# Optimization experiments

Measured on AMD Instinct MI355X. Metric: run time of the kernel, lower is better.

## Reference

```python
import jax, jax.numpy as jnp
import numpy as np
import math

N = 8192
DIM = 256

def setup_inputs() -> dict:
    key = jax.random.key(0)
    k1, k2, k3 = jax.random.split(key, 3)
    h = jax.random.normal(k1, (N, DIM), dtype=jnp.float32)
    # xavier_uniform with gain=1.414 for square [dim, dim] matrices
    gain = 1.414
    bound = gain * math.sqrt(6.0 / (DIM + DIM))
    Wq = jax.random.uniform(k2, (DIM, DIM), dtype=jnp.float32, minval=-bound, maxval=bound)
    Wk = jax.random.uniform(k3, (DIM, DIM), dtype=jnp.float32, minval=-bound, maxval=bound)
    return {"h": h, "Wq": Wq, "Wk": Wk}

def reference(h, Wq, Wk):
    dim = h.shape[1]
    q = h @ Wq                                   # [N, dim]
    k = h @ Wk                                   # [N, dim]
    e = (q @ k.T) / jnp.sqrt(jnp.asarray(dim, h.dtype))  # [N, N]
    attention = jax.nn.softmax(e, axis=1)        # row-wise softmax
    attention = attention.mean(axis=0)           # [N], column-mean over rows
    x = attention @ h                            # [dim]
    return x
```

## Files before the change

kernel.cpp:

```cpp
#include <hip/hip_runtime.h>
#include <cstdint>
#include <cstddef>


#define N_ROWS 8192
#define DIM    256

typedef __bf16 bf16x8 __attribute__((ext_vector_type(8)));
typedef unsigned short u16x8 __attribute__((ext_vector_type(8)));
typedef float f32x16 __attribute__((ext_vector_type(16)));

__device__ __forceinline__ uint16_t f2bf(float f) {
    uint32_t u = __float_as_uint(f);
    uint32_t r = (u + 0x7fffu + ((u >> 16) & 1u)) >> 16;
    return (uint16_t)r;
}

__device__ __forceinline__ float fexp2(float x) {
#if __has_builtin(__builtin_amdgcn_exp2f)
    return __builtin_amdgcn_exp2f(x);
#else
    return __expf(x * 0.69314718056f);
#endif
}

__device__ __forceinline__ void gld16(const void* gsrc, void* ldst) {
    __builtin_amdgcn_global_load_lds(
        (const __attribute__((address_space(1))) unsigned int*)gsrc,
        (__attribute__((address_space(3))) unsigned int*)ldst, 16, 0, 0);
}

__global__ __launch_bounds__(256) void proj_kernel(
        const float* __restrict__ h, const float* __restrict__ Wq,
        const float* __restrict__ Wk, uint16_t* __restrict__ qf,
        uint16_t* __restrict__ kf, float* __restrict__ l_arr,
        float* __restrict__ c_arr, float* __restrict__ out) {
    __shared__ alignas(16) uint16_t wb[256 * 128];
    const int tid = threadIdx.x, lane = tid & 63, wave = tid >> 6;
    const int which = blockIdx.x & 1;
    const int rt = blockIdx.x >> 1;

    if (blockIdx.x < 32)       l_arr[blockIdx.x * 256 + tid] = 0.0f;
    else if (blockIdx.x < 64)  c_arr[(blockIdx.x - 32) * 256 + tid] = 0.0f;
    else if (blockIdx.x == 64) out[tid] = 0.0f;

    const float* __restrict__ W = which ? Wk : Wq;
    uint16_t* __restrict__ dst = which ? kf : qf;
    const float scale = which ? 1.0f : (0.0625f * 1.44269504089f);

    {
        float* hb = (float*)wb;
        for (int i = tid; i < 2048; i += 256) {
            int r = i >> 6, c = (i & 63) * 4;
            float4 v = *(const float4*)&h[(size_t)(rt * 32 + r) * DIM + c];
            *(float4*)&hb[r * 260 + c] = v;
        }
    }
    __syncthreads();

    bf16x8 afrag[16];
    {
        const float* hb = (const float*)wb;
        const int r = lane & 31;
#pragma unroll
        for (int a0 = 0; a0 < 16; a0++) {
            const int c0 = a0 * 16 + (lane >> 5) * 8;
            float4 f0 = *(const float4*)&hb[r * 260 + c0];
            float4 f1 = *(const float4*)&hb[r * 260 + c0 + 4];
            u16x8 f;
            f[0] = f2bf(f0.x); f[1] = f2bf(f0.y); f[2] = f2bf(f0.z); f[3] = f2bf(f0.w);
            f[4] = f2bf(f1.x); f[5] = f2bf(f1.y); f[6] = f2bf(f1.z); f[7] = f2bf(f1.w);
            afrag[a0] = __builtin_bit_cast(bf16x8, f);
        }
    }

    for (int p = 0; p < 2; p++) {
        __syncthreads();
#pragma unroll
        for (int c = 0; c < 32; c++) {
            int f = c * 256 + tid;
            int k = f >> 5, nc = (f & 31) * 4;
            float4 w4 = *(const float4*)&W[(size_t)k * DIM + p * 128 + nc];
            ushort4 b;
            b.x = f2bf(w4.x); b.y = f2bf(w4.y); b.z = f2bf(w4.z); b.w = f2bf(w4.w);
            *(ushort4*)&wb[k * 128 + nc] = b;
        }
        __syncthreads();

        f32x16 acc;
#pragma unroll
        for (int i = 0; i < 16; i++) acc[i] = 0.0f;
        const int cl = wave * 32 + (lane & 31);
#pragma unroll
        for (int a0 = 0; a0 < 16; a0++) {
            const int kb = a0 * 16 + (lane >> 5) * 8;
            u16x8 f;
#pragma unroll
            for (int j = 0; j < 8; j++) f[j] = wb[(kb + j) * 128 + cl];
            acc = __builtin_amdgcn_mfma_f32_32x32x16_bf16(
                afrag[a0], __builtin_bit_cast(bf16x8, f), acc, 0, 0, 0);
        }
        __syncthreads();

        {
            uint16_t* rp = &wb[wave * 2048];
            const int dcl = lane & 31;
            const int a0o = dcl >> 4, hi = (dcl >> 3) & 1, j = dcl & 7;
            const int ilb = 4 * (lane >> 5);
#pragma unroll
            for (int reg = 0; reg < 16; reg++) {
                int il = ilb + (reg & 3) + 8 * (reg >> 2);
                rp[(size_t)((a0o * 64) + il + 32 * hi) * 8 + j] =
                    f2bf(acc[reg] * scale);
            }
            const uint4* rv = (const uint4*)rp;
            uint4* gp = (uint4*)(dst + (size_t)rt * 8192 +
                                 (size_t)(p * 8 + wave * 2) * 512);
            gp[lane * 2]     = rv[lane * 2];
            gp[lane * 2 + 1] = rv[lane * 2 + 1];
        }
    }
}

template <int MODE>
__global__ __launch_bounds__(256, 2) void qk_pass(
        const uint16_t* __restrict__ qf, const uint16_t* __restrict__ kf,
        float* __restrict__ l_arr, float* __restrict__ c_arr) {
    __shared__ alignas(16) uint16_t ktile[2][8192];
    __shared__ float c_lds[512];
    const int tid = threadIdx.x, lane = tid & 63, wave = tid >> 6;
    const int bid = blockIdx.x;
    const int cc = bid & 15, rb = bid >> 4;
    const int t0 = rb * 8 + wave * 2;
    const int row0 = t0 * 32;

    const uint4* qp = (const uint4*)qf;
    bf16x8 q0[16], q1[16];
#pragma unroll
    for (int a0 = 0; a0 < 16; a0++) {
        q0[a0] = __builtin_bit_cast(bf16x8, qp[(size_t)t0 * 1024 + a0 * 64 + lane]);
        q1[a0] = __builtin_bit_cast(bf16x8, qp[(size_t)(t0 + 1) * 1024 + a0 * 64 + lane]);
    }

    float rs0[16], rs1[16];
    float rr0[16], rr1[16];
    if (MODE == 0) {
#pragma unroll
        for (int r = 0; r < 16; r++) { rs0[r] = 0.0f; rs1[r] = 0.0f; }
    } else {
#pragma unroll
        for (int r = 0; r < 16; r++) {
            int ro = (r & 3) + 8 * (r >> 2) + 4 * (lane >> 5);
            rr0[r] = 1.0f / (8192.0f * l_arr[row0 + ro]);
            rr1[r] = 1.0f / (8192.0f * l_arr[row0 + 32 + ro]);
        }
        for (int i = tid; i < 512; i += 256) c_lds[i] = 0.0f;
    }

    const char* ksrc = (const char*)kf + (size_t)cc * 16 * 16384;

    {
        const char* s0 = ksrc + wave * 4096 + lane * 16;
        char* d0 = (char*)&ktile[0][0] + wave * 4096;
#pragma unroll
        for (int it = 0; it < 4; it++) gld16(s0 + it * 1024, d0 + it * 1024);
    }

    for (int t = 0; t < 16; t++) {
        __syncthreads();
        if (t < 15) {
            const char* sn = ksrc + (t + 1) * 16384 + wave * 4096 + lane * 16;
            char* dn = (char*)&ktile[(t + 1) & 1][0] + wave * 4096;
#pragma unroll
            for (int it = 0; it < 4; it++) gld16(sn + it * 1024, dn + it * 1024);
        }

        const uint16_t* kt = &ktile[t & 1][0];
        f32x16 acc0, acc1;
#pragma unroll
        for (int i = 0; i < 16; i++) { acc0[i] = 0.0f; acc1[i] = 0.0f; }
#pragma unroll
        for (int a0 = 0; a0 < 16; a0++) {
            bf16x8 b = __builtin_bit_cast(bf16x8,
                *(const u16x8*)&kt[(size_t)(a0 * 64 + lane) * 8]);
            acc0 = __builtin_amdgcn_mfma_f32_32x32x16_bf16(q0[a0], b, acc0, 0, 0, 0);
            acc1 = __builtin_amdgcn_mfma_f32_32x32x16_bf16(q1[a0], b, acc1, 0, 0, 0);
        }

        if (MODE == 0) {
#pragma unroll
            for (int r = 0; r < 16; r++) {
                rs0[r] += fexp2(acc0[r]);
                rs1[r] += fexp2(acc1[r]);
            }
        } else {
            float sv = 0.0f;
#pragma unroll
            for (int r = 0; r < 16; r++) {
                sv += fexp2(acc0[r]) * rr0[r];
                sv += fexp2(acc1[r]) * rr1[r];
            }
            sv += __shfl_xor(sv, 32);
            if (lane < 32) atomicAdd(&c_lds[t * 32 + lane], sv);
        }
    }

    if (MODE == 0) {
#pragma unroll
        for (int r = 0; r < 16; r++) {
            float v0 = rs0[r], v1 = rs1[r];
            v0 += __shfl_xor(v0, 1);  v0 += __shfl_xor(v0, 2);
            v0 += __shfl_xor(v0, 4);  v0 += __shfl_xor(v0, 8);
            v0 += __shfl_xor(v0, 16);
            v1 += __shfl_xor(v1, 1);  v1 += __shfl_xor(v1, 2);
            v1 += __shfl_xor(v1, 4);  v1 += __shfl_xor(v1, 8);
            v1 += __shfl_xor(v1, 16);
            if ((lane & 31) == 0) {
                int ro = (r & 3) + 8 * (r >> 2) + 4 * (lane >> 5);
                atomicAdd(&l_arr[row0 + ro], v0);
                atomicAdd(&l_arr[row0 + 32 + ro], v1);
            }
        }
    } else {
        __syncthreads();
        for (int i = tid; i < 512; i += 256)
            atomicAdd(&c_arr[cc * 512 + i], c_lds[i]);
    }
}

__global__ __launch_bounds__(256) void finish_kernel(
        const float* __restrict__ h, const float* __restrict__ c_arr,
        float* __restrict__ out) {
    const int d = threadIdx.x;
    const int j0 = blockIdx.x * 64;
    float acc = 0.0f;
    for (int j = j0; j < j0 + 64; j++) acc += c_arr[j] * h[(size_t)j * DIM + d];
    atomicAdd(&out[d], acc);
}

extern "C" void kernel_launch(void* const* d_in, const int* in_sizes, int n_in,
                              void* d_out, int out_size, void* d_ws, size_t ws_size,
                              hipStream_t stream) {
    const float* h  = (const float*)d_in[0];
    const float* Wq = (const float*)d_in[1];
    const float* Wk = (const float*)d_in[2];

    uint16_t* qf = (uint16_t*)d_ws;
    uint16_t* kf = qf + (size_t)N_ROWS * DIM;
    float* l_arr = (float*)((char*)d_ws + (size_t)8 * 1024 * 1024);
    float* c_arr = l_arr + N_ROWS;
    float* out = (float*)d_out;

    proj_kernel<<<512, 256, 0, stream>>>(h, Wq, Wk, qf, kf, l_arr, c_arr, out);
    qk_pass<0><<<512, 256, 0, stream>>>(qf, kf, l_arr, c_arr);
    qk_pass<1><<<512, 256, 0, stream>>>(qf, kf, l_arr, c_arr);
    finish_kernel<<<128, 256, 0, stream>>>(h, c_arr, out);
}
```

Before: 162.5 us.

## Restructure projection kernel to compute Q and K per block with direct W loads

The projection kernel now uses 128 blocks that each cover 64 rows of h, converting h to bf16 once in shared memory. Each block computes both the Q and K projections, and waves read W straight from global memory with per-element bf16 conversion instead of staging W through LDS with barriers. This cuts repeated h loads and barriers but replaces coalesced W staging with strided scalar global reads that rely on the cache. The finish kernel is also split into 256 blocks of 32 rows with an unrolled loop to raise parallelism.

```diff
diff --git a/kernel.cpp b/kernel.cpp
--- a/kernel.cpp
+++ b/kernel.cpp
@@ -35,87 +35,68 @@
         const float* __restrict__ Wk, uint16_t* __restrict__ qf,
         uint16_t* __restrict__ kf, float* __restrict__ l_arr,
         float* __restrict__ c_arr, float* __restrict__ out) {
-    __shared__ alignas(16) uint16_t wb[256 * 128];
+    __shared__ alignas(16) uint16_t hb16[64 * 264];
+    __shared__ alignas(16) uint16_t rep[4][1024];
     const int tid = threadIdx.x, lane = tid & 63, wave = tid >> 6;
-    const int which = blockIdx.x & 1;
-    const int rt = blockIdx.x >> 1;
-
-    if (blockIdx.x < 32)       l_arr[blockIdx.x * 256 + tid] = 0.0f;
-    else if (blockIdx.x < 64)  c_arr[(blockIdx.x - 32) * 256 + tid] = 0.0f;
-    else if (blockIdx.x == 64) out[tid] = 0.0f;
-
-    const float* __restrict__ W = which ? Wk : Wq;
-    uint16_t* __restrict__ dst = which ? kf : qf;
-    const float scale = which ? 1.0f : (0.0625f * 1.44269504089f);
-
-    {
-        float* hb = (float*)wb;
-        for (int i = tid; i < 2048; i += 256) {
-            int r = i >> 6, c = (i & 63) * 4;
-            float4 v = *(const float4*)&h[(size_t)(rt * 32 + r) * DIM + c];
-            *(float4*)&hb[r * 260 + c] = v;
-        }
+    const int bid = blockIdx.x;
+
+    if (bid < 32)       l_arr[bid * 256 + tid] = 0.0f;
+    else if (bid < 64)  c_arr[(bid - 32) * 256 + tid] = 0.0f;
+    else if (bid == 64) out[tid] = 0.0f;
+
+    for (int i = tid; i < 4096; i += 256) {
+        int r = i >> 6, c4 = (i & 63) * 4;
+        float4 v = *(const float4*)&h[(size_t)(bid * 64 + r) * DIM + c4];
+        ushort4 b;
+        b.x = f2bf(v.x); b.y = f2bf(v.y); b.z = f2bf(v.z); b.w = f2bf(v.w);
+        *(ushort4*)&hb16[r * 264 + c4] = b;
     }
     __syncthreads();
 
     bf16x8 afrag[16];
-    {
-        const float* hb = (const float*)wb;
-        const int r = lane & 31;
-#pragma unroll
-        for (int a0 = 0; a0 < 16; a0++) {
-            const int c0 = a0 * 16 + (lane >> 5) * 8;
-            float4 f0 = *(const float4*)&hb[r * 260 + c0];
-            float4 f1 = *(const float4*)&hb[r * 260 + c0 + 4];
-            u16x8 f;
-            f[0] = f2bf(f0.x); f[1] = f2bf(f0.y); f[2] = f2bf(f0.z); f[3] = f2bf(f0.w);
-            f[4] = f2bf(f1.x); f[5] = f2bf(f1.y); f[6] = f2bf(f1.z); f[7] = f2bf(f1.w);
-            afrag[a0] = __builtin_bit_cast(bf16x8, f);
-        }
-    }
-
-    for (int p = 0; p < 2; p++) {
-        __syncthreads();
-#pragma unroll
-        for (int c = 0; c < 32; c++) {
-            int f = c * 256 + tid;
-            int k = f >> 5, nc = (f & 31) * 4;
-            float4 w4 = *(const float4*)&W[(size_t)k * DIM + p * 128 + nc];
-            ushort4 b;
-            b.x = f2bf(w4.x); b.y = f2bf(w4.y); b.z = f2bf(w4.z); b.w = f2bf(w4.w);
-            *(ushort4*)&wb[k * 128 + nc] = b;
-        }
-        __syncthreads();
-
-        f32x16 acc;
-#pragma unroll
-        for (int i = 0; i < 16; i++) acc[i] = 0.0f;
-        const int cl = wave * 32 + (lane & 31);
-#pragma unroll
-        for (int a0 = 0; a0 < 16; a0++) {
-            const int kb = a0 * 16 + (lane >> 5) * 8;
-            u16x8 f;
-#pragma unroll
-            for (int j = 0; j < 8; j++) f[j] = wb[(kb + j) * 128 + cl];
-            acc = __builtin_amdgcn_mfma_f32_32x32x16_bf16(
-                afrag[a0], __builtin_bit_cast(bf16x8, f), acc, 0, 0, 0);
-        }
-        __syncthreads();
-
-        {
-            uint16_t* rp = &wb[wave * 2048];
+    const int lr = (wave >> 1) * 32 + (lane & 31);
+#pragma unroll
+    for (int a0 = 0; a0 < 16; a0++) {
+        int c0 = a0 * 16 + (lane >> 5) * 8;
+        afrag[a0] = __builtin_bit_cast(bf16x8, *(const u16x8*)&hb16[lr * 264 + c0]);
+    }
+    const int rtg = bid * 2 + (wave >> 1);
+
+#pragma unroll 1
+    for (int ph = 0; ph < 4; ph++) {
+        const int which = ph >> 1, p = ph & 1;
+        const float* __restrict__ W = which ? Wk : Wq;
+        uint16_t* __restrict__ dst = which ? kf : qf;
+        const float scale = which ? 1.0f : (0.0625f * 1.44269504089f);
+#pragma unroll
+        for (int cti = 0; cti < 2; cti++) {
+            const int ctl = (wave & 1) * 2 + cti;
+            const int cl = ctl * 32 + (lane & 31);
+            f32x16 acc;
+#pragma unroll
+            for (int i = 0; i < 16; i++) acc[i] = 0.0f;
+#pragma unroll
+            for (int a0 = 0; a0 < 16; a0++) {
+                const int kb = a0 * 16 + (lane >> 5) * 8;
+                u16x8 f;
+#pragma unroll
+                for (int j = 0; j < 8; j++)
+                    f[j] = f2bf(W[(size_t)(kb + j) * DIM + p * 128 + cl]);
+                acc = __builtin_amdgcn_mfma_f32_32x32x16_bf16(
+                    afrag[a0], __builtin_bit_cast(bf16x8, f), acc, 0, 0, 0);
+            }
             const int dcl = lane & 31;
-            const int a0o = dcl >> 4, hi = (dcl >> 3) & 1, j = dcl & 7;
+            const int a0o = dcl >> 4, hi = (dcl >> 3) & 1, jj = dcl & 7;
             const int ilb = 4 * (lane >> 5);
 #pragma unroll
             for (int reg = 0; reg < 16; reg++) {
                 int il = ilb + (reg & 3) + 8 * (reg >> 2);
-                rp[(size_t)((a0o * 64) + il + 32 * hi) * 8 + j] =
+                rep[wave][(size_t)((a0o * 64) + il + 32 * hi) * 8 + jj] =
                     f2bf(acc[reg] * scale);
             }
-            const uint4* rv = (const uint4*)rp;
-            uint4* gp = (uint4*)(dst + (size_t)rt * 8192 +
-                                 (size_t)(p * 8 + wave * 2) * 512);
+            const uint4* rv = (const uint4*)&rep[wave][0];
+            uint4* gp = (uint4*)(dst + (size_t)rtg * 8192 +
+                                 (size_t)(p * 8 + ctl * 2) * 512);
             gp[lane * 2]     = rv[lane * 2];
             gp[lane * 2 + 1] = rv[lane * 2 + 1];
         }
@@ -232,9 +213,11 @@
         const float* __restrict__ h, const float* __restrict__ c_arr,
         float* __restrict__ out) {
     const int d = threadIdx.x;
-    const int j0 = blockIdx.x * 64;
+    const int j0 = blockIdx.x * 32;
     float acc = 0.0f;
-    for (int j = j0; j < j0 + 64; j++) acc += c_arr[j] * h[(size_t)j * DIM + d];
+#pragma unroll
+    for (int jj = 0; jj < 32; jj++)
+        acc += c_arr[j0 + jj] * h[(size_t)(j0 + jj) * DIM + d];
     atomicAdd(&out[d], acc);
 }
 
@@ -251,8 +234,8 @@
     float* c_arr = l_arr + N_ROWS;
     float* out = (float*)d_out;
 
-    proj_kernel<<<512, 256, 0, stream>>>(h, Wq, Wk, qf, kf, l_arr, c_arr, out);
+    proj_kernel<<<128, 256, 0, stream>>>(h, Wq, Wk, qf, kf, l_arr, c_arr, out);
     qk_pass<0><<<512, 256, 0, stream>>>(qf, kf, l_arr, c_arr);
     qk_pass<1><<<512, 256, 0, stream>>>(qf, kf, l_arr, c_arr);
-    finish_kernel<<<128, 256, 0, stream>>>(h, c_arr, out);
-}
+    finish_kernel<<<256, 256, 0, stream>>>(h, c_arr, out);
+}
```

Result: slower. 200.7 us (+23.6%).
